# Kernel optimization log

Measured on AMD Instinct MI355X. Metric: run time of the kernel, lower is better.

Reference implementation:

```python
import jax, jax.numpy as jnp
import numpy as np

B = 16384       # batch of peptide samples
M = 15          # max_peptide_size
R = 64          # aa_rep_size
P = 34          # number of pocket positions
F = 9           # filter_size
A = 20          # alphabet size


def setup_inputs() -> dict:
    key = jax.random.key(0)
    k1, k2, k3, k4 = jax.random.split(key, 4)
    peptide_encoding = jax.random.normal(k1, (B, M, R), dtype=jnp.float32)
    pocket_aa_idx = jax.random.randint(k2, (B, P), 0, A, dtype=jnp.int32)
    adj_mask = jax.random.randint(k3, (B, P, M), 0, 2, dtype=jnp.int32)
    # one trainable 1-D filter of length F per alphabet letter ('uniform' init)
    kernels = jax.random.uniform(k4, (A, F), dtype=jnp.float32, minval=-0.05, maxval=0.05)
    return {"peptide_encoding": peptide_encoding, "pocket_aa_idx": pocket_aa_idx,
            "adj_mask": adj_mask, "kernels": kernels}


def reference(peptide_encoding, pocket_aa_idx, adj_mask, kernels):
    # Per pocket position p of sample b: filter = kernels[pocket_aa_idx[b,p]]  [B,P,F]
    filt = kernels[pocket_aa_idx]
    # Convolution is linear, so sum the adjacent peptide-position encodings first:
    # s[b,p,r] = sum_m adj_mask[b,p,m] * peptide_encoding[b,m,r]   -> [B,P,R]
    s = jnp.einsum('bpm,bmr->bpr', adj_mask.astype(peptide_encoding.dtype), peptide_encoding)
    # Full convolution along the representation axis: output length R + F - 1
    conv1 = jax.vmap(jax.vmap(lambda a, b: jnp.convolve(a, b, mode='full')))
    out = conv1(s, filt)  # [B, P, R+F-1]
    return out
```

## Files before the change

### kernel.cpp

```cpp
#include <hip/hip_runtime.h>

#define MM 15
#define RR 64
#define PP 34
#define FF 9
#define AA 20
#define OW 72
#define SP 84
#define KS 12
#define AJ 16

__global__ __launch_bounds__(256)
void ppc_kernel(const float* __restrict__ pe,
                const int*   __restrict__ idx,
                const int*   __restrict__ adj,
                const float* __restrict__ kernels,
                float*       __restrict__ out)
{
    const int b = blockIdx.x;
    const int t = threadIdx.x;

    __shared__ float s_kern[AA * KS];
    __shared__ float s_adjf[PP * AJ];
    __shared__ int   s_idx[PP];
    __shared__ float s_s[PP * SP];

    const float* peb  = pe  + (size_t)b * (MM * RR);
    const int*   adjb = adj + (size_t)b * (PP * MM);

    const int w    = t >> 6;
    const int lane = t & 63;

    float pv[MM];
    #pragma unroll
    for (int m = 0; m < MM; ++m) pv[m] = peb[m * RR + lane];

    if (t < AA * FF) {
        int a = (unsigned)t / FF, j = t - a * FF;
        s_kern[a * KS + j] = kernels[t];
    }
    for (int i = t; i < PP * MM; i += 256) {
        int p = (unsigned)i / MM, m = i - p * MM;
        s_adjf[p * AJ + m] = (float)adjb[i];
    }
    if (t < PP) s_idx[t] = idx[(size_t)b * PP + t];
    if (t < PP * 5) {
        int p = (unsigned)t / 5, k = t - p * 5;
        int off = p * SP + (k < 2 ? k * 4 : 72 + (k - 2) * 4);
        *(float4*)&s_s[off] = make_float4(0.f, 0.f, 0.f, 0.f);
    }
    __syncthreads();

    #pragma unroll
    for (int j = 0; j < 9; ++j) {
        const int p = w + 4 * j;
        if (p < PP) {
            const float* g = &s_adjf[p * AJ];
            const float4 g0 = *(const float4*)&g[0];
            const float4 g1 = *(const float4*)&g[4];
            const float4 g2 = *(const float4*)&g[8];
            const float4 g3 = *(const float4*)&g[12];
            float acc;
            acc  = g0.x * pv[0]  + g0.y * pv[1]  + g0.z * pv[2]  + g0.w * pv[3];
            acc += g1.x * pv[4]  + g1.y * pv[5]  + g1.z * pv[6]  + g1.w * pv[7];
            acc += g2.x * pv[8]  + g2.y * pv[9]  + g2.z * pv[10] + g2.w * pv[11];
            acc += g3.x * pv[12] + g3.y * pv[13] + g3.z * pv[14];
            s_s[p * SP + 8 + lane] = acc;
        }
    }

    float* outb = out + (size_t)b * (PP * OW);

    const int rowk = (unsigned)lane / 18u;
    const int q18  = lane - 18 * rowk;
    const int o0   = q18 << 2;

    #pragma unroll
    for (int k = 0; k < 3; ++k) {
        const int j = 3 * k + rowk;
        const int p = w + 4 * j;
        if (rowk < 3 && p < PP) {
            const float* kb = &s_kern[s_idx[p] * KS];
            const float4 k0 = *(const float4*)&kb[0];
            const float4 k1 = *(const float4*)&kb[4];
            float kf[FF];
            kf[0]=k0.x; kf[1]=k0.y; kf[2]=k0.z; kf[3]=k0.w;
            kf[4]=k1.x; kf[5]=k1.y; kf[6]=k1.z; kf[7]=k1.w;
            kf[8]=kb[8];

            const float* row = &s_s[p * SP];
            float wv[12];
            *(float4*)&wv[0] = *(const float4*)&row[o0];
            *(float4*)&wv[4] = *(const float4*)&row[o0 + 4];
            *(float4*)&wv[8] = *(const float4*)&row[o0 + 8];

            float ax=0, ay=0, az=0, aw=0;
            #pragma unroll
            for (int jj = 0; jj < FF; ++jj) {
                const float kk = kf[jj];
                ax += kk * wv[8  - jj];
                ay += kk * wv[9  - jj];
                az += kk * wv[10 - jj];
                aw += kk * wv[11 - jj];
            }
            *(float4*)&outb[p * OW + o0] = make_float4(ax, ay, az, aw);
        }
    }
}

extern "C" void kernel_launch(void* const* d_in, const int* in_sizes, int n_in,
                              void* d_out, int out_size, void* d_ws, size_t ws_size,
                              hipStream_t stream) {
    const float* pe      = (const float*)d_in[0];
    const int*   idx     = (const int*)  d_in[1];
    const int*   adj     = (const int*)  d_in[2];
    const float* kernels = (const float*)d_in[3];
    float*       out     = (float*)d_out;

    const int B = in_sizes[0] / (MM * RR);
    ppc_kernel<<<B, 256, 0, stream>>>(pe, idx, adj, kernels, out);
}
```

Measured before the change: 73.72 us.

## Remove block barrier by making each wave self-sufficient and reading adj via scalar loads

Drops the shared adjacency staging and the block-wide __syncthreads. Each wavefront now writes its own copy of the filter table and pocket indices, zeroes the padding only for the rows it owns, and reads adj_mask straight from global memory. Because the row index is wave-uniform, those adj reads can become scalar loads, and the mask is used as a branch-select add instead of a multiply. An explicit lgkmcnt wait stands in for the barrier, since each wave reads back only the LDS data it wrote itself. The intent is to remove barrier stalls and LDS staging so waves can overlap freely, at the cost of redundant per-wave writes of the filter table and more scalar global traffic.

```diff
diff --git a/kernel.cpp b/kernel.cpp
--- a/kernel.cpp
+++ b/kernel.cpp
@@ -8,7 +8,6 @@
 #define OW 72
 #define SP 84
 #define KS 12
-#define AJ 16
 
 __global__ __launch_bounds__(256)
 void ppc_kernel(const float* __restrict__ pe,
@@ -17,76 +16,67 @@
                 const float* __restrict__ kernels,
                 float*       __restrict__ out)
 {
-    const int b = blockIdx.x;
-    const int t = threadIdx.x;
+    const int b    = blockIdx.x;
+    const int t    = threadIdx.x;
+    const int lane = t & 63;
+    const int w    = __builtin_amdgcn_readfirstlane(t >> 6);
 
     __shared__ float s_kern[AA * KS];
-    __shared__ float s_adjf[PP * AJ];
     __shared__ int   s_idx[PP];
     __shared__ float s_s[PP * SP];
 
-    const float* peb  = pe  + (size_t)b * (MM * RR);
-    const int*   adjb = adj + (size_t)b * (PP * MM);
-
-    const int w    = t >> 6;
-    const int lane = t & 63;
+    const float* peb = pe + (size_t)b * (MM * RR);
 
     float pv[MM];
     #pragma unroll
     for (int m = 0; m < MM; ++m) pv[m] = peb[m * RR + lane];
 
-    if (t < AA * FF) {
-        int a = (unsigned)t / FF, j = t - a * FF;
-        s_kern[a * KS + j] = kernels[t];
+    if (lane < 60) {
+        #pragma unroll
+        for (int u = 0; u < 3; ++u) {
+            const int i = lane * 3 + u;
+            const int a = (unsigned)i / FF, j = i - a * FF;
+            s_kern[a * KS + j] = kernels[i];
+        }
     }
-    for (int i = t; i < PP * MM; i += 256) {
-        int p = (unsigned)i / MM, m = i - p * MM;
-        s_adjf[p * AJ + m] = (float)adjb[i];
+    if (lane < PP) s_idx[lane] = idx[(size_t)b * PP + lane];
+    if (lane < 45) {
+        const int j  = (unsigned)lane / 5, kk = lane - j * 5;
+        const int p  = w + 4 * j;
+        if (p < PP) {
+            const int off = p * SP + (kk < 2 ? kk * 4 : 72 + (kk - 2) * 4);
+            *(float4*)&s_s[off] = make_float4(0.f, 0.f, 0.f, 0.f);
+        }
     }
-    if (t < PP) s_idx[t] = idx[(size_t)b * PP + t];
-    if (t < PP * 5) {
-        int p = (unsigned)t / 5, k = t - p * 5;
-        int off = p * SP + (k < 2 ? k * 4 : 72 + (k - 2) * 4);
-        *(float4*)&s_s[off] = make_float4(0.f, 0.f, 0.f, 0.f);
-    }
-    __syncthreads();
 
+    const int* adjb = adj + (size_t)b * (PP * MM);
     #pragma unroll
     for (int j = 0; j < 9; ++j) {
         const int p = w + 4 * j;
         if (p < PP) {
-            const float* g = &s_adjf[p * AJ];
-            const float4 g0 = *(const float4*)&g[0];
-            const float4 g1 = *(const float4*)&g[4];
-            const float4 g2 = *(const float4*)&g[8];
-            const float4 g3 = *(const float4*)&g[12];
-            float acc;
-            acc  = g0.x * pv[0]  + g0.y * pv[1]  + g0.z * pv[2]  + g0.w * pv[3];
-            acc += g1.x * pv[4]  + g1.y * pv[5]  + g1.z * pv[6]  + g1.w * pv[7];
-            acc += g2.x * pv[8]  + g2.y * pv[9]  + g2.z * pv[10] + g2.w * pv[11];
-            acc += g3.x * pv[12] + g3.y * pv[13] + g3.z * pv[14];
+            const int* g = adjb + p * MM;
+            float acc = 0.f;
+            #pragma unroll
+            for (int m = 0; m < MM; ++m)
+                if (g[m] != 0) acc += pv[m];
             s_s[p * SP + 8 + lane] = acc;
         }
     }
 
+    asm volatile("s_waitcnt lgkmcnt(0)" ::: "memory");
+
     float* outb = out + (size_t)b * (PP * OW);
-
     const int rowk = (unsigned)lane / 18u;
-    const int q18  = lane - 18 * rowk;
-    const int o0   = q18 << 2;
+    const int o0   = (lane - 18 * rowk) << 2;
 
     #pragma unroll
     for (int k = 0; k < 3; ++k) {
-        const int j = 3 * k + rowk;
-        const int p = w + 4 * j;
+        const int p = w + 12 * k + 4 * rowk;
         if (rowk < 3 && p < PP) {
             const float* kb = &s_kern[s_idx[p] * KS];
             const float4 k0 = *(const float4*)&kb[0];
             const float4 k1 = *(const float4*)&kb[4];
-            float kf[FF];
-            kf[0]=k0.x; kf[1]=k0.y; kf[2]=k0.z; kf[3]=k0.w;
-            kf[4]=k1.x; kf[5]=k1.y; kf[6]=k1.z; kf[7]=k1.w;
-            kf[8]=kb[8];
+            float kf[FF] = {k0.x,k0.y,k0.z,k0.w, k1.x,k1.y,k1.z,k1.w, kb[8]};
 
             const float* row = &s_s[p * SP];
             float wv[12];
```

Result: no change. 73.77 us (+0.1%).
